# Kernel tuning notes

Hardware: AMD Instinct MI355X
Metric: run time of the kernel (lower is better)

## Reference

```python
import jax, jax.numpy as jnp
import numpy as np


def conv(x, w, b=None, pad=1):
    y = jax.lax.conv_general_dilated(x, w, (1, 1), [(pad, pad), (pad, pad)],
                                     dimension_numbers=('NCHW', 'OIHW', 'NCHW'))
    if b is not None:
        y = y + b[None, :, None, None]
    return y


def grid_sample(img, gx, gy):
    # bilinear, zeros padding, align_corners=False (torch F.grid_sample default)
    B, C, H, W = img.shape
    ix = ((gx + 1.0) * W - 1.0) * 0.5
    iy = ((gy + 1.0) * H - 1.0) * 0.5
    x0 = jnp.floor(ix)
    y0 = jnp.floor(iy)

    def gather(xi, yi):
        valid = (xi >= 0) & (xi <= W - 1) & (yi >= 0) & (yi <= H - 1)
        xc = jnp.clip(xi, 0, W - 1).astype(jnp.int32)
        yc = jnp.clip(yi, 0, H - 1).astype(jnp.int32)
        b = jnp.arange(B)[:, None, None]
        return img[b, :, yc, xc] * valid[..., None].astype(img.dtype)  # (B,H,W,C)

    wx1 = ix - x0
    wy1 = iy - y0
    wx0 = 1.0 - wx1
    wy0 = 1.0 - wy1
    out = (gather(x0, y0) * (wx0 * wy0)[..., None]
           + gather(x0 + 1, y0) * (wx1 * wy0)[..., None]
           + gather(x0, y0 + 1) * (wx0 * wy1)[..., None]
           + gather(x0 + 1, y0 + 1) * (wx1 * wy1)[..., None])
    return out.transpose(0, 3, 1, 2)  # (B,C,H,W)


def setup_inputs() -> dict:
    key = jax.random.key(0)
    ks = jax.random.split(key, 32)
    B, H, W, hd = 4, 512, 512, 16
    f = lambda k, shp: jax.random.normal(k, shp, dtype=jnp.float32) * 0.05
    z = lambda n: jnp.zeros((n,), dtype=jnp.float32)
    d = {
        'net': f(ks[0], (B, hd, H, W)),
        'inp': f(ks[1], (B, hd, H, W)),
        'corr': f(ks[2], (B, 3, H, W)),
        'noise': f(ks[3], (B, 3, H, W)),
        # BasicMotionEncoder (channels=3, hidden=32, output_dim=64)
        'wc1': f(ks[4], (32, 3, 3, 3)), 'bc1': z(32),
        'wc2': f(ks[5], (32, 32, 3, 3)), 'bc2': z(32),
        'wf1': f(ks[6], (32, 3, 3, 3)), 'bf1': z(32),
        'wf2': f(ks[7], (32, 32, 3, 3)), 'bf2': z(32),
        'we': f(ks[8], (61, 64, 3, 3)), 'be': z(61),
        # SepConvGRU (hidden_size=16, L=4)
        'loc1_w': f(ks[9], (16, 96, 5, 5)), 'loc1_b': z(16),
        'loc2_w': f(ks[10], (8, 16, 5, 5)), 'loc2_b': z(8),
        'wz': f(ks[11], (16, 144, 3, 3)), 'bz': z(16),
        'wr': f(ks[12], (16, 144, 3, 3)), 'br': z(16),
        'wq': f(ks[13], (16, 96, 3, 3)), 'bq': z(16),
        # CBAM (reduction 16 -> mid=1; bias-free, standard impl)
        'ca_w1': f(ks[14], (1, 16, 1, 1)),
        'ca_w2': f(ks[15], (16, 1, 1, 1)),
        'sa_w': f(ks[16], (1, 2, 7, 7)),
        # FlowHead (input 16, hidden 64, out 3)
        'fh1_w': f(ks[17], (64, 16, 3, 3)), 'fh1_b': z(64),
        'fh2_w': f(ks[18], (3, 64, 3, 3)), 'fh2_b': z(3),
    }
    return d


def reference(net, inp, corr, noise, wc1, bc1, wc2, bc2, wf1, bf1, wf2, bf2, we, be,
              loc1_w, loc1_b, loc2_w, loc2_b, wz, bz, wr, br, wq, bq,
              ca_w1, ca_w2, sa_w, fh1_w, fh1_b, fh2_w, fh2_b):
    # --- BasicMotionEncoder ---
    cor = jax.nn.relu(conv(corr, wc1, bc1, 1))
    cor = jax.nn.relu(conv(cor, wc2, bc2, 1))
    flo = jax.nn.relu(conv(noise, wf1, bf1, 1))
    flo = jax.nn.relu(conv(flo, wf2, bf2, 1))
    mo = jax.nn.relu(conv(jnp.concatenate([cor, flo], 1), we, be, 1))
    motion = jnp.concatenate([mo, noise], 1)  # (B,64,H,W)
    x = jnp.concatenate([inp, motion], 1)     # (B,hd+64,H,W)
    h = net
    B, C, H, W = h.shape
    # --- SepConvGRU ---
    t = jax.nn.leaky_relu(conv(jnp.concatenate([x, h], 1), loc1_w, loc1_b, 2), 0.2)
    flows = conv(t, loc2_w, loc2_b, 2)        # (B,2L,H,W)
    L = flows.shape[1] // 2
    flows = flows.reshape(B, L, 2, H, W)
    xx = jnp.arange(W, dtype=h.dtype)[None, None, :]  # (1,1,W)
    yy = jnp.arange(H, dtype=h.dtype)[None, :, None]  # (1,H,1)

    def warp_one(flow):  # flow: (B,2,H,W); warp h by -flow
        vgx = xx - flow[:, 0]
        vgy = yy - flow[:, 1]
        gx = 2.0 * vgx / max(W - 1, 1) - 1.0
        gy = 2.0 * vgy / max(H - 1, 1) - 1.0
        return grid_sample(h, gx, gy)

    wrapped = jax.vmap(warp_one, in_axes=1, out_axes=1)(flows)  # (B,L,C,H,W)
    wrapped = wrapped.reshape(B, L * C, H, W)
    hx = jnp.concatenate([wrapped, x], 1)     # (B,9*hd,H,W)
    zg = jax.nn.sigmoid(conv(hx, wz, bz, 1))
    rg = jax.nn.sigmoid(conv(hx, wr, br, 1))
    q = jnp.tanh(conv(jnp.concatenate([rg * h, x], 1), wq, bq, 1))
    h = (1.0 - zg) * h + zg * q
    # --- CBAM ---
    avg = h.mean((2, 3), keepdims=True)
    mx = h.max((2, 3), keepdims=True)
    mlp = lambda v: conv(jax.nn.relu(conv(v, ca_w1, None, 0)), ca_w2, None, 0)
    h = h * jax.nn.sigmoid(mlp(avg) + mlp(mx))
    sa = jnp.concatenate([h.mean(1, keepdims=True), h.max(1, keepdims=True)], 1)
    h = h * jax.nn.sigmoid(conv(sa, sa_w, None, 3))
    # --- FlowHead ---
    delta_flow = conv(jax.nn.relu(conv(h, fh1_w, fh1_b, 1)), fh2_w, fh2_b, 1)
    return h, delta_flow
```

## Files before the change

### kernel.cpp

```cpp
#include <hip/hip_runtime.h>
#include <hip/hip_bf16.h>
#include <math.h>

using bf16 = __hip_bfloat16;
typedef __attribute__((ext_vector_type(8))) short short8;
typedef __attribute__((ext_vector_type(4))) float f32x4;

__device__ __forceinline__ float b2f(bf16 v){ return __bfloat162float(v); }
__device__ __forceinline__ bf16 f2b(float v){ return __float2bfloat16(v); }
__device__ __forceinline__ float bs2f(short s){
  union{unsigned u; float f;} x; x.u = ((unsigned)(unsigned short)s)<<16; return x.f;
}
__device__ __forceinline__ float lo16(unsigned u){ union{unsigned x; float f;} v; v.x = u<<16;          return v.f; }
__device__ __forceinline__ float hi16(unsigned u){ union{unsigned x; float f;} v; v.x = u & 0xffff0000u; return v.f; }
__device__ __forceinline__ unsigned cvt_pk_bf16(float lo, float hi){
  unsigned r; asm("v_cvt_pk_bf16_f32 %0, %1, %2" : "=v"(r) : "v"(lo), "v"(hi)); return r;
}
__device__ __forceinline__ float hw_exp2(float x){ float r; asm("v_exp_f32 %0, %1" : "=v"(r) : "v"(x)); return r; }
__device__ __forceinline__ float hw_rcp(float x){ float r; asm("v_rcp_f32 %0, %1" : "=v"(r) : "v"(x)); return r; }
__device__ __forceinline__ float fast_sigmoid(float v){ return hw_rcp(1.f + hw_exp2(v * -1.44269504f)); }
__device__ __forceinline__ float fast_tanh(float v){ return 1.f - 2.f*hw_rcp(1.f + hw_exp2(v * 2.88539008f)); }

template<int A> __device__ __forceinline__ float act_fn(float v){
  if constexpr (A==1) return fmaxf(v, 0.f);
  else if constexpr (A==2) return v > 0.f ? v : 0.2f*v;
  else if constexpr (A==3) return fast_sigmoid(v);
  else if constexpr (A==4) return fast_tanh(v);
  else return v;
}

struct Srcs9 { const bf16* p[9]; int code[9]; };

template<int KK, int ACT, int NT>
__global__ __launch_bounds__(256) void conv_mfma(
    Srcs9 S, int Gin, const bf16* __restrict__ flows,
    const bf16* __restrict__ Bw, const float* __restrict__ bias,
    bf16* __restrict__ outS, size_t slabS, float* __restrict__ outF, int Cout,
    int H, int W)
{
  constexpr int TS=16, HALO=TS+KK-1, PAD=KK/2, NPAIR=(KK*KK+1)/2, HH=HALO*HALO;
  constexpr int CP=24, CPB=48;
  constexpr int NMT = (NT==1)?4:((NT==2)?8:16);
  __shared__ __align__(16) bf16 As[HH*CP];
  const int tid=threadIdx.x, lane=tid&63, wv=tid>>6;
  const int ln=lane&15, gq=lane>>4;
  const int tilesx=W/TS;
  const int nwg = gridDim.x, cpx = nwg >> 3;
  const int bidx = (blockIdx.x & 7)*cpx + (blockIdx.x >> 3);
  const int tx0 = (bidx % tilesx)*TS, ty0 = (bidx / tilesx)*TS;
  const int b=blockIdx.z; const int HW=H*W;
  int ntile, mt0;
  if constexpr (NT==1){ ntile=0;    mt0=wv*4; }
  else if constexpr (NT==2){ ntile=wv&1; mt0=(wv>>1)*8; }
  else { ntile=wv; mt0=0; }

  f32x4 acc[NMT];
  #pragma unroll
  for (int t=0;t<NMT;++t) acc[t]=(f32x4){0.f,0.f,0.f,0.f};

  const short8 Z8 = {0,0,0,0,0,0,0,0};
  const int px0=tid, px1=tid+256;
  const int hy0=px0/HALO, hx0=px0-hy0*HALO;
  const int hy1=px1/HALO, hx1=px1-hy1*HALO;
  const bool act1 = (px1<HH);
  const int gy0=ty0+hy0-PAD, gx0=tx0+hx0-PAD;
  const int gy1=ty0+hy1-PAD, gx1=tx0+hx1-PAD;
  const bool in0 = (gy0>=0&&gy0<H&&gx0>=0&&gx0<W);
  const bool in1 = act1 && (gy1>=0&&gy1<H&&gx1>=0&&gx1<W);
  const size_t po0 = ((size_t)b*HW + (size_t)(in0?gy0:0)*W + (in0?gx0:0))*16;
  const size_t po1 = ((size_t)b*HW + (size_t)(in1?gy1:0)*W + (in1?gx1:0))*16;

  auto gather = [&](int g, bool inb, size_t po, int gy, int gx, short8& A0, short8& A1){
    const int code = S.code[g];
    const bf16* sp = S.p[g];
    if (code == 0) {
      if (inb) {
        const bf16* qp = sp + po;
        A0 = *(const short8*)qp; A1 = *(const short8*)(qp+8);
      } else { A0 = Z8; A1 = Z8; }
    } else {
      if (inb) {
        const int l = code-1;
        const unsigned fp_ = *(const unsigned*)(flows + po + 2*l);
        const float fx = lo16(fp_), fy = hi16(fp_);
        const float vgx = (float)gx - fx, vgy = (float)gy - fy;
        const float gxn = 2.f*vgx/(float)(W-1) - 1.f;
        const float gyn = 2.f*vgy/(float)(H-1) - 1.f;
        const float ix = ((gxn+1.f)*(float)W - 1.f)*0.5f;
        const float iy = ((gyn+1.f)*(float)H - 1.f)*0.5f;
        const float x0f = floorf(ix), y0f = floorf(iy);
        const float wx1 = ix-x0f, wy1 = iy-y0f, wx0 = 1.f-wx1, wy0 = 1.f-wy1;
        const int x0=(int)x0f, y0=(int)y0f, x1=x0+1, y1=y0+1;
        const bool vx0=(x0>=0)&(x0<W), vx1=(x1>=0)&(x1<W);
        const bool vy0=(y0>=0)&(y0<H), vy1=(y1>=0)&(y1<H);
        const int xc0=min(max(x0,0),W-1), xc1=min(max(x1,0),W-1);
        const int yc0=min(max(y0,0),H-1), yc1=min(max(y1,0),H-1);
        const float w00=wx0*wy0*((vx0&&vy0)?1.f:0.f);
        const float w10=wx1*wy0*((vx1&&vy0)?1.f:0.f);
        const float w01=wx0*wy1*((vx0&&vy1)?1.f:0.f);
        const float w11=wx1*wy1*((vx1&&vy1)?1.f:0.f);
        const bf16* nb = sp + (size_t)b*HW*16;
        const bf16* p00 = nb + ((size_t)yc0*W+xc0)*16;
        const bf16* p10 = nb + ((size_t)yc0*W+xc1)*16;
        const bf16* p01 = nb + ((size_t)yc1*W+xc0)*16;
        const bf16* p11 = nb + ((size_t)yc1*W+xc1)*16;
        unsigned t00[8], t10[8], t01[8], t11[8], od[8];
        *(uint4*)t00     = *(const uint4*)p00; *(uint4*)(t00+4) = *(const uint4*)(p00+8);
        *(uint4*)t10     = *(const uint4*)p10; *(uint4*)(t10+4) = *(const uint4*)(p10+8);
        *(uint4*)t01     = *(const uint4*)p01; *(uint4*)(t01+4) = *(const uint4*)(p01+8);
        *(uint4*)t11     = *(const uint4*)p11; *(uint4*)(t11+4) = *(const uint4*)(p11+8);
        #pragma unroll
        for (int j=0;j<8;++j){
          const float lo = w00*lo16(t00[j]) + w10*lo16(t10[j]) + w01*lo16(t01[j]) + w11*lo16(t11[j]);
          const float hi = w00*hi16(t00[j]) + w10*hi16(t10[j]) + w01*hi16(t01[j]) + w11*hi16(t11[j]);
          od[j] = cvt_pk_bf16(lo, hi);
        }
        A0 = *(const short8*)od; A1 = *(const short8*)(od+4);
      } else { A0 = Z8; A1 = Z8; }
    }
  };

  auto mfma_g = [&](int g){
    const bf16* bw = Bw + ((size_t)g*NPAIR*NT + ntile)*512;
    const char* bufm = (const char*)As + (size_t)mt0*(HALO*CPB);
    #pragma unroll
    for (int p=0;p<NPAIR;++p){
      const short8 bfrag = *(const short8*)(bw + (size_t)p*(NT*512) + lane*8);
      int off = 2*p + (gq>>1);
      if (off >= KK*KK) off = 0;
      const int dy = off/KK, dx = off - (off/KK)*KK;
      const int ce = (dy*HALO + ln + dx)*CPB + ((gq&1)<<4);
      #pragma unroll
      for (int t=0;t<NMT;++t){
        const short8 af = *(const short8*)(bufm + (size_t)t*(HALO*CPB) + ce);
        acc[t] = __builtin_amdgcn_mfma_f32_16x16x32_bf16(af, bfrag, acc[t], 0, 0, 0);
      }
    }
  };

  for (int g=0; g<Gin; ++g) {
    short8 a0, a1, c0v, c1v;
    gather(g, in0, po0, gy0, gx0, a0, a1);
    if (act1) gather(g, in1, po1, gy1, gx1, c0v, c1v);
    if (g > 0) { mfma_g(g-1); __syncthreads(); }
    *(short8*)(As + (size_t)px0*CP)     = a0;
    *(short8*)(As + (size_t)px0*CP + 8) = a1;
    if (act1){
      *(short8*)(As + (size_t)px1*CP)     = c0v;
      *(short8*)(As + (size_t)px1*CP + 8) = c1v;
    }
    __syncthreads();
  }
  mfma_g(Gin-1);

  const int co = ntile*16 + ln;
  const float bv = bias[co];
  if (outS) {
    #pragma unroll
    for (int t=0;t<NMT;++t){
      const int y = ty0 + mt0 + t;
      bf16* op = outS + (size_t)ntile*slabS + ((size_t)b*HW + (size_t)y*W + tx0 + gq*4)*16 + ln;
      const float f0 = act_fn<ACT>(acc[t][0] + bv);
      const float f1 = act_fn<ACT>(acc[t][1] + bv);
      const float f2 = act_fn<ACT>(acc[t][2] + bv);
      const float f3 = act_fn<ACT>(acc[t][3] + bv);
      const unsigned p01 = cvt_pk_bf16(f0, f1), p23 = cvt_pk_bf16(f2, f3);
      unsigned short* os = (unsigned short*)op;
      os[0]  = (unsigned short)p01; os[16] = (unsigned short)(p01>>16);
      os[32] = (unsigned short)p23; os[48] = (unsigned short)(p23>>16);
    }
  } else {
    if (co < Cout) {
      #pragma unroll
      for (int t=0;t<NMT;++t){
        const int y = ty0 + mt0 + t;
        float4 f;
        f.x = act_fn<ACT>(acc[t][0]+bv); f.y = act_fn<ACT>(acc[t][1]+bv);
        f.z = act_fn<ACT>(acc[t][2]+bv); f.w = act_fn<ACT>(acc[t][3]+bv);
        *(float4*)(outF + ((size_t)b*Cout + co)*HW + (size_t)y*W + tx0 + gq*4) = f;
      }
    }
  }
}

struct PrepDesc {
  const float *W1, *W2, *b1, *b2;
  int coSplit, NPAIR, NTp, Cout, CinO, T;
  int lo0, hi0, d2, lo2, hi2;
  int base[9];
  int total;
};
struct PrepAll { PrepDesc d[10]; int n; };

__global__ void prep_w(PrepAll P, bf16* __restrict__ Bw, float* __restrict__ bOut, int grand){
  const int i = blockIdx.x*256 + threadIdx.x;
  if (i < P.n*64) {
    const int c=i>>6, t=i&63; const PrepDesc& D=P.d[c];
    float bv=0.f;
    if (t < D.Cout) bv = (!D.b2 || t < D.coSplit) ? D.b1[t] : D.b2[t-D.coSplit];
    bOut[c*64+t]=bv;
  }
  if (i >= grand) return;
  int c=0, off0=0;
  while (i >= off0 + P.d[c].total) { off0 += P.d[c].total; ++c; }
  const PrepDesc& D = P.d[c];
  const int j = i - off0;
  const int jj=j&7, l=(j>>3)&63, ln2=l&15, gq2=l>>4;
  int r=j>>9; const int nt=r%D.NTp; r/=D.NTp; const int p=r%D.NPAIR; const int g=r/D.NPAIR;
  const int k=gq2*8+jj, off=2*p+(k>>4), ci=k&15, co=nt*16+ln2;
  float w=0.f;
  if (off<D.T && co<D.Cout) {
    const int lo = (g==0)?D.lo0:0, hi=(g==0)?D.hi0:16;
    if (!D.W2 || co < D.coSplit) {
      if (ci>=lo && ci<hi) w = D.W1[((size_t)co*D.CinO + D.base[g]+ci)*D.T + off];
    } else {
      if (ci>=D.lo2 && ci<D.hi2) w = D.W2[((size_t)(co-D.coSplit)*D.CinO + D.base[g]+ci+D.d2)*D.T + off];
    }
  }
  Bw[i] = f2b(w);
}

__global__ void pack_all(const float* __restrict__ corr, const float* __restrict__ noise,
                         const float* __restrict__ inp, const float* __restrict__ net,
                         bf16* __restrict__ cnoise, bf16* __restrict__ inpT,
                         bf16* __restrict__ netT, int HW){
  const int px = blockIdx.x*256+threadIdx.x; const int b=blockIdx.y;
  if (px>=HW) return;
  const size_t base = ((size_t)b*HW+px)*16;
  __align__(16) bf16 t[16];
  #pragma unroll
  for (int c=0;c<16;++c) t[c]=f2b(0.f);
  #pragma unroll
  for (int c=0;c<3;++c){
    t[c]   = f2b(corr [((size_t)b*3+c)*HW+px]);
    t[3+c] = f2b(noise[((size_t)b*3+c)*HW+px]);
  }
  *(short8*)(cnoise+base) = *(const short8*)t; *(short8*)(cnoise+base+8) = *(const short8*)(t+8);
  #pragma unroll
  for (int c=0;c<16;++c) t[c]=f2b(inp[((size_t)b*16+c)*HW+px]);
  *(short8*)(inpT+base) = *(const short8*)t; *(short8*)(inpT+base+8) = *(const short8*)(t+8);
  #pragma unroll
  for (int c=0;c<16;++c) t[c]=f2b(net[((size_t)b*16+c)*HW+px]);
  *(short8*)(netT+base) = *(const short8*)t; *(short8*)(netT+base+8) = *(const short8*)(t+8);
}

__global__ void noise_tail(const float* __restrict__ noise, bf16* __restrict__ mslab3, int HW){
  const int px = blockIdx.x*256+threadIdx.x; const int b=blockIdx.y;
  if (px>=HW) return;
  bf16* d = mslab3 + ((size_t)b*HW+px)*16;
  #pragma unroll
  for (int c=0;c<3;++c) d[13+c] = f2b(noise[((size_t)b*3+c)*HW+px]);
}

__global__ void rh_k(const bf16* __restrict__ rg, const bf16* __restrict__ netT,
                     bf16* __restrict__ rh, int HW){
  const int px = blockIdx.x*256+threadIdx.x; const int b=blockIdx.y;
  if (px>=HW) return;
  const size_t base = ((size_t)b*HW+px)*16;
  const short8 r0=*(const short8*)(rg+base),  r1=*(const short8*)(rg+base+8);
  const short8 n0=*(const short8*)(netT+base), n1=*(const short8*)(netT+base+8);
  __align__(16) bf16 t[16];
  #pragma unroll
  for (int c=0;c<8;++c){
    t[c]   = f2b(bs2f(r0[c])*bs2f(n0[c]));
    t[8+c] = f2b(bs2f(r1[c])*bs2f(n1[c]));
  }
  *(short8*)(rh+base) = *(const short8*)t; *(short8*)(rh+base+8) = *(const short8*)(t+8);
}

__global__ void h1_k(const bf16* __restrict__ zg, const bf16* __restrict__ q,
                     const float* __restrict__ net, bf16* __restrict__ hT, int HW){
  const int px = blockIdx.x*256+threadIdx.x; const int b=blockIdx.y;
  if (px>=HW) return;
  const size_t base = ((size_t)b*HW+px)*16;
  const short8 z0=*(const short8*)(zg+base), z1=*(const short8*)(zg+base+8);
  const short8 q0=*(const short8*)(q+base),  q1=*(const short8*)(q+base+8);
  __align__(16) bf16 t[16];
  #pragma unroll
  for (int c=0;c<8;++c){
    const float za=bs2f(z0[c]), zb=bs2f(z1[c]);
    const float na=net[((size_t)b*16+c)*HW+px], nb2=net[((size_t)b*16+8+c)*HW+px];
    t[c]   = f2b((1.f-za)*na + za*bs2f(q0[c]));
    t[8+c] = f2b((1.f-zb)*nb2 + zb*bs2f(q1[c]));
  }
  *(short8*)(hT+base) = *(const short8*)t; *(short8*)(hT+base+8) = *(const short8*)(t+8);
}

__global__ __launch_bounds__(256) void castats_p1(const bf16* __restrict__ hT,
                                                  float* __restrict__ part, int HW){
  const int blk=blockIdx.x, b=blockIdx.y;
  const int per = HW>>5;
  const bf16* base = hT + ((size_t)b*HW + (size_t)blk*per)*16;
  float s[16], m[16];
  #pragma unroll
  for (int c=0;c<16;++c){ s[c]=0.f; m[c]=-3.4e38f; }
  for (int i=threadIdx.x;i<per;i+=256){
    const short8 a=*(const short8*)(base+(size_t)i*16);
    const short8 bb=*(const short8*)(base+(size_t)i*16+8);
    #pragma unroll
    for (int c=0;c<8;++c){
      const float v=bs2f(a[c]);  s[c]+=v;   m[c]=fmaxf(m[c],v);
      const float w=bs2f(bb[c]); s[8+c]+=w; m[8+c]=fmaxf(m[8+c],w);
    }
  }
  #pragma unroll
  for (int o=32;o>=1;o>>=1){
    #pragma unroll
    for (int c=0;c<16;++c){ s[c]+=__shfl_down(s[c],o); m[c]=fmaxf(m[c],__shfl_down(m[c],o)); }
  }
  __shared__ float ls[4][16], lm[4][16];
  const int w4=threadIdx.x>>6;
  if ((threadIdx.x&63)==0){
    #pragma unroll
    for (int c=0;c<16;++c){ ls[w4][c]=s[c]; lm[w4][c]=m[c]; }
  }
  __syncthreads();
  if (threadIdx.x<16){
    const int c=threadIdx.x;
    part[((size_t)(b*32+blk))*32 + c]      = ls[0][c]+ls[1][c]+ls[2][c]+ls[3][c];
    part[((size_t)(b*32+blk))*32 + 16 + c] = fmaxf(fmaxf(lm[0][c],lm[1][c]),fmaxf(lm[2][c],lm[3][c]));
  }
}

__global__ void castats_fin(const float* __restrict__ part, const float* __restrict__ w1,
                            const float* __restrict__ w2, float* __restrict__ scale, int HW){
  const int t = threadIdx.x; if (t>=64) return;
  const int b=t>>4, c=t&15;
  float s=0.f, m=-3.4e38f;
  for (int k=0;k<32;++k){
    s += part[((size_t)(b*32+k))*32 + c];
    m  = fmaxf(m, part[((size_t)(b*32+k))*32 + 16 + c]);
  }
  float pa = w1[c]*(s/(float)HW), pm = w1[c]*m;
  #pragma unroll
  for (int o=8;o>=1;o>>=1){ pa += __shfl_xor(pa,o,16); pm += __shfl_xor(pm,o,16); }
  const float y = w2[c]*fmaxf(pa,0.f) + w2[c]*fmaxf(pm,0.f);
  scale[t] = fast_sigmoid(y);
}

__global__ void sastats_k(const bf16* __restrict__ hT, const float* __restrict__ scale,
                          bf16* __restrict__ sa2, int HW){
  const int px = blockIdx.x*256+threadIdx.x; const int b=blockIdx.y;
  if (px>=HW) return;
  const size_t base = ((size_t)b*HW+px)*16;
  const short8 a=*(const short8*)(hT+base), c8=*(const short8*)(hT+base+8);
  float s=0.f, m=-3.4e38f;
  #pragma unroll
  for (int c=0;c<8;++c){
    const float v=bs2f(a[c])*scale[b*16+c];    s+=v; m=fmaxf(m,v);
    const float w=bs2f(c8[c])*scale[b*16+8+c]; s+=w; m=fmaxf(m,w);
  }
  sa2[((size_t)b*2+0)*HW+px] = f2b(s*(1.f/16.f));
  sa2[((size_t)b*2+1)*HW+px] = f2b(m);
}

__global__ __launch_bounds__(256) void hfinal2(bf16* __restrict__ hT, const float* __restrict__ scale,
    const bf16* __restrict__ sa2, const float* __restrict__ saw,
    float* __restrict__ outh, int H, int W){
  __shared__ float wl[98];
  if (threadIdx.x < 98) wl[threadIdx.x] = saw[threadIdx.x];
  __syncthreads();
  const int i = blockIdx.x*256 + threadIdx.x; const int b = blockIdx.y;
  const int HW = H*W;
  if (i >= HW) return;
  const int y = i / W, x = i - (i/W)*W;
  float s = 0.f;
  #pragma unroll
  for (int ch=0; ch<2; ++ch){
    const size_t base = ((size_t)b*2+ch)*HW;
    for (int ky=0;ky<7;++ky){
      const int yy=y+ky-3; if (yy<0||yy>=H) continue;
      for (int kx=0;kx<7;++kx){
        const int xx=x+kx-3; if (xx<0||xx>=W) continue;
        s += b2f(sa2[base+(size_t)yy*W+xx]) * wl[ch*49+ky*7+kx];
      }
    }
  }
  const float sa = fast_sigmoid(s);
  const size_t base = ((size_t)b*HW+i)*16;
  const short8 a=*(const short8*)(hT+base), c8=*(const short8*)(hT+base+8);
  __align__(16) bf16 t[16];
  #pragma unroll
  for (int c=0;c<8;++c){
    const float v=bs2f(a[c])*scale[b*16+c]*sa;
    const float w=bs2f(c8[c])*scale[b*16+8+c]*sa;
    t[c]=f2b(v); t[8+c]=f2b(w);
    outh[((size_t)b*16+c)*HW+i]=v; outh[((size_t)b*16+8+c)*HW+i]=w;
  }
  *(short8*)(hT+base)=*(const short8*)t; *(short8*)(hT+base+8)=*(const short8*)(t+8);
}

extern "C" void kernel_launch(void* const* d_in, const int* in_sizes, int n_in,
                              void* d_out, int out_size, void* d_ws, size_t ws_size,
                              hipStream_t stream)
{
  const float* net   = (const float*)d_in[0];
  const float* inp   = (const float*)d_in[1];
  const float* corr  = (const float*)d_in[2];
  const float* noise = (const float*)d_in[3];
  const float* wc1 = (const float*)d_in[4];  const float* bc1 = (const float*)d_in[5];
  const float* wc2 = (const float*)d_in[6];  const float* bc2 = (const float*)d_in[7];
  const float* wf1 = (const float*)d_in[8];  const float* bf1 = (const float*)d_in[9];
  const float* wf2 = (const float*)d_in[10]; const float* bf2 = (const float*)d_in[11];
  const float* we  = (const float*)d_in[12]; const float* be  = (const float*)d_in[13];
  const float* loc1_w = (const float*)d_in[14]; const float* loc1_b = (const float*)d_in[15];
  const float* loc2_w = (const float*)d_in[16]; const float* loc2_b = (const float*)d_in[17];
  const float* wz = (const float*)d_in[18]; const float* bz = (const float*)d_in[19];
  const float* wr = (const float*)d_in[20]; const float* br = (const float*)d_in[21];
  const float* wq = (const float*)d_in[22]; const float* bq = (const float*)d_in[23];
  const float* ca_w1 = (const float*)d_in[24]; const float* ca_w2 = (const float*)d_in[25];
  const float* sa_w  = (const float*)d_in[26];
  const float* fh1_w = (const float*)d_in[27]; const float* fh1_b = (const float*)d_in[28];
  const float* fh2_w = (const float*)d_in[29]; const float* fh2_b = (const float*)d_in[30];

  const int B = 4, H = 512, W = 512, HW = H*W;
  const size_t U  = 32ull<<20;
  const size_t SS = (size_t)B*HW*16;
  char* ws = (char*)d_ws;

  bf16* cor1   = (bf16*)(ws + 0*U);
  bf16* flo1   = (bf16*)(ws + 2*U);
  bf16* motion = (bf16*)(ws + 0*U);
  bf16* fh1o   = (bf16*)(ws + 0*U);
  bf16* inpT   = (bf16*)(ws + 4*U);
  bf16* flo2   = (bf16*)(ws + 5*U);
  bf16* flows  = (bf16*)(ws + 5*U);
  bf16* qb     = (bf16*)(ws + 5*U);
  bf16* cnoise = (bf16*)(ws + 6*U);
  bf16* tbuf   = (bf16*)(ws + 6*U);
  bf16* rh     = (bf16*)(ws + 6*U);
  bf16* hT     = (bf16*)(ws + 6*U);
  bf16* netT   = (bf16*)(ws + 7*U);
  float* part    = (float*)(ws + 4*U);
  float* scale   = (float*)(ws + 4*U + (64<<10));
  bf16*  sa2     = (bf16*)(ws + 4*U + (1<<20));
  bf16*  Bw_fh2  = (bf16*)(ws + 4*U + (16<<20));
  float* bias_fh2= (float*)(ws + 4*U + (17<<20));

  float* out_h  = (float*)d_out;
  float* out_df = out_h + (size_t)B*16*HW;
  bf16*  zgrg   = (bf16*)d_out;
  bf16*  BwAll  = (bf16*)out_df;
  float* biasAll= (float*)(BwAll + 190464);

  const size_t oMrg=0, oCor2=10240, oFlo2=20480, oMo=30720, oLoc1=71680,
               oLoc2=111616, oZgrg=118272, oQ=164352, oFh1=179712;
  const int grand = 189952;

  const dim3 pgrid((HW+255)/256, B);
  const dim3 cgrid((W/16)*(H/16), 1, B);

  auto mk = [](const float* W1, const float* W2, int coSplit, const float* b1, const float* b2,
               int G, int NP, int NTp, int Cout, int CinO, int T,
               int lo0, int hi0, int d2, int lo2, int hi2,
               int b0,int b1_,int b2_,int b3,int b4,int b5,int b6,int b7,int b8)->PrepDesc{
    PrepDesc d{};
    d.W1=W1; d.W2=W2; d.b1=b1; d.b2=b2; d.coSplit=coSplit;
    d.NPAIR=NP; d.NTp=NTp; d.Cout=Cout; d.CinO=CinO; d.T=T;
    d.lo0=lo0; d.hi0=hi0; d.d2=d2; d.lo2=lo2; d.hi2=hi2;
    const int bs[9]={b0,b1_,b2_,b3,b4,b5,b6,b7,b8};
    for (int g=0;g<9;++g) d.base[g]=bs[g];
    d.total = G*NP*NTp*512;
    return d;
  };

  {
    PrepAll P{}; P.n = 9;
    P.d[0] = mk(wc1, wf1, 32, bc1, bf1, 1,5,4, 64,3,9,  0,3, -3,3,6, 0,0,0,0,0,0,0,0,0);
    P.d[1] = mk(wc2, nullptr,0, bc2,nullptr, 2,5,2, 32,32,9, 0,16, 0,0,16, 0,16,0,0,0,0,0,0,0);
    P.d[2] = mk(wf2, nullptr,0, bf2,nullptr, 2,5,2, 32,32,9, 0,16, 0,0,16, 0,16,0,0,0,0,0,0,0);
    P.d[3] = mk(we,  nullptr,0, be, nullptr, 4,5,4, 61,64,9, 0,16, 0,0,16, 0,16,32,48,0,0,0,0,0);
    P.d[4] = mk(loc1_w,nullptr,0, loc1_b,nullptr, 6,13,1, 16,96,25, 0,16, 0,0,16, 0,16,32,48,64,80,0,0,0);
    P.d[5] = mk(loc2_w,nullptr,0, loc2_b,nullptr, 1,13,1, 8,16,25,  0,16, 0,0,16, 0,0,0,0,0,0,0,0,0);
    P.d[6] = mk(wz, wr, 16, bz, br, 9,5,2, 32,144,9, 0,16, 0,0,16, 0,16,32,48,64,80,96,112,128);
    P.d[7] = mk(wq, nullptr,0, bq, nullptr, 6,5,1, 16,96,9, 0,16, 0,0,16, 0,16,32,48,64,80,0,0,0);
    P.d[8] = mk(fh1_w,nullptr,0, fh1_b,nullptr, 1,5,4, 64,16,9, 0,16, 0,0,16, 0,0,0,0,0,0,0,0,0);
    prep_w<<<(grand+255)/256,256,0,stream>>>(P, BwAll, biasAll, grand);
  }

  pack_all<<<pgrid,256,0,stream>>>(corr, noise, inp, net, cnoise, inpT, netT, HW);

  { Srcs9 S{}; S.p[0]=cnoise;
    conv_mfma<3,1,4><<<cgrid,256,0,stream>>>(S,1,nullptr,BwAll+oMrg,biasAll+0*64,cor1,SS,nullptr,64,H,W); }
  { Srcs9 S{}; S.p[0]=cor1; S.p[1]=cor1+SS;
    conv_mfma<3,1,2><<<cgrid,256,0,stream>>>(S,2,nullptr,BwAll+oCor2,biasAll+1*64,zgrg,SS,nullptr,32,H,W); }
  { Srcs9 S{}; S.p[0]=flo1; S.p[1]=flo1+SS;
    conv_mfma<3,1,2><<<cgrid,256,0,stream>>>(S,2,nullptr,BwAll+oFlo2,biasAll+2*64,flo2,SS,nullptr,32,H,W); }
  { Srcs9 S{}; S.p[0]=zgrg; S.p[1]=zgrg+SS; S.p[2]=flo2; S.p[3]=flo2+SS;
    conv_mfma<3,1,4><<<cgrid,256,0,stream>>>(S,4,nullptr,BwAll+oMo,biasAll+3*64,motion,SS,nullptr,61,H,W); }
  noise_tail<<<pgrid,256,0,stream>>>(noise, motion+3*SS, HW);

  { Srcs9 S{}; S.p[0]=inpT; S.p[1]=motion; S.p[2]=motion+SS; S.p[3]=motion+2*SS; S.p[4]=motion+3*SS; S.p[5]=netT;
    conv_mfma<5,2,1><<<cgrid,256,0,stream>>>(S,6,nullptr,BwAll+oLoc1,biasAll+4*64,tbuf,SS,nullptr,16,H,W); }
  { Srcs9 S{}; S.p[0]=tbuf;
    conv_mfma<5,0,1><<<cgrid,256,0,stream>>>(S,1,nullptr,BwAll+oLoc2,biasAll+5*64,flows,SS,nullptr,8,H,W); }

  { Srcs9 S{};
    S.p[0]=netT; S.code[0]=1; S.p[1]=netT; S.code[1]=2;
    S.p[2]=netT; S.code[2]=3; S.p[3]=netT; S.code[3]=4;
    S.p[4]=inpT; S.p[5]=motion; S.p[6]=motion+SS; S.p[7]=motion+2*SS; S.p[8]=motion+3*SS;
    conv_mfma<3,3,2><<<cgrid,256,0,stream>>>(S,9,flows,BwAll+oZgrg,biasAll+6*64,zgrg,SS,nullptr,32,H,W); }
  rh_k<<<pgrid,256,0,stream>>>(zgrg+SS, netT, rh, HW);
  { Srcs9 S{}; S.p[0]=rh; S.p[1]=inpT; S.p[2]=motion; S.p[3]=motion+SS; S.p[4]=motion+2*SS; S.p[5]=motion+3*SS;
    conv_mfma<3,4,1><<<cgrid,256,0,stream>>>(S,6,nullptr,BwAll+oQ,biasAll+7*64,qb,SS,nullptr,16,H,W); }
  h1_k<<<pgrid,256,0,stream>>>(zgrg, qb, net, hT, HW);

  { PrepAll P{}; P.n = 1;
    P.d[0] = mk(fh2_w,nullptr,0, fh2_b,nullptr, 4,5,1, 3,64,9, 0,16, 0,0,16, 0,16,32,48,0,0,0,0,0);
    prep_w<<<(10240+255)/256,256,0,stream>>>(P, Bw_fh2, bias_fh2, 10240); }

  castats_p1<<<dim3(32,B),256,0,stream>>>(hT, part, HW);
  castats_fin<<<1,64,0,stream>>>(part, ca_w1, ca_w2, scale, HW);
  sastats_k<<<pgrid,256,0,stream>>>(hT, scale, sa2, HW);
  hfinal2<<<pgrid,256,0,stream>>>(hT, scale, sa2, sa_w, out_h, H, W);

  { Srcs9 S{}; S.p[0]=hT;
    conv_mfma<3,1,4><<<cgrid,256,0,stream>>>(S,1,nullptr,BwAll+oFh1,biasAll+8*64,fh1o,SS,nullptr,64,H,W); }
  { Srcs9 S{}; S.p[0]=fh1o; S.p[1]=fh1o+SS; S.p[2]=fh1o+2*SS; S.p[3]=fh1o+3*SS;
    conv_mfma<3,0,1><<<cgrid,256,0,stream>>>(S,4,nullptr,Bw_fh2,bias_fh2,nullptr,SS,out_df,3,H,W); }
}
```

Measured before the change: 896.4 us.

## Fuse r*h into q-conv gather, merge weight prep with packing, read bf16 net

Removes the standalone rh_k kernel by adding a gather mode that multiplies the reset gate by the hidden state while loading the q-conv input halo. Merges the weight-prep and input-pack kernels into one launch that uses an extra grid row. h1_k now reads the packed bf16 net instead of strided fp32 net. This saves launches and one full-resolution write/read round trip, at the cost of recomputing the product for halo pixels and slightly different rounding of net in h1.

```diff
diff --git a/kernel.cpp b/kernel.cpp
--- a/kernel.cpp
+++ b/kernel.cpp
@@ -33,7 +33,7 @@
 
 template<int KK, int ACT, int NT>
 __global__ __launch_bounds__(256) void conv_mfma(
-    Srcs9 S, int Gin, const bf16* __restrict__ flows,
+    Srcs9 S, int Gin, const bf16* __restrict__ flows, const bf16* __restrict__ rgp,
     const bf16* __restrict__ Bw, const float* __restrict__ bias,
     bf16* __restrict__ outS, size_t slabS, float* __restrict__ outF, int Cout,
     int H, int W)
@@ -77,6 +77,16 @@
       if (inb) {
         const bf16* qp = sp + po;
         A0 = *(const short8*)qp; A1 = *(const short8*)(qp+8);
+      } else { A0 = Z8; A1 = Z8; }
+    } else if (code == 5) {
+      if (inb) {
+        unsigned nu[8], ru[8], od[8];
+        *(uint4*)nu     = *(const uint4*)(sp + po);  *(uint4*)(nu+4) = *(const uint4*)(sp + po + 8);
+        *(uint4*)ru     = *(const uint4*)(rgp + po); *(uint4*)(ru+4) = *(const uint4*)(rgp + po + 8);
+        #pragma unroll
+        for (int j=0;j<8;++j)
+          od[j] = cvt_pk_bf16(lo16(nu[j])*lo16(ru[j]), hi16(nu[j])*hi16(ru[j]));
+        A0 = *(const short8*)od; A1 = *(const short8*)(od+4);
       } else { A0 = Z8; A1 = Z8; }
     } else {
       if (inb) {
@@ -192,8 +202,8 @@
 };
 struct PrepAll { PrepDesc d[10]; int n; };
 
-__global__ void prep_w(PrepAll P, bf16* __restrict__ Bw, float* __restrict__ bOut, int grand){
-  const int i = blockIdx.x*256 + threadIdx.x;
+__device__ __forceinline__ void prep_body(const PrepAll& P, bf16* Bw, float* bOut,
+                                          int grand, int i){
   if (i < P.n*64) {
     const int c=i>>6, t=i&63; const PrepDesc& D=P.d[c];
     float bv=0.f;
@@ -220,11 +230,19 @@
   Bw[i] = f2b(w);
 }
 
-__global__ void pack_all(const float* __restrict__ corr, const float* __restrict__ noise,
-                         const float* __restrict__ inp, const float* __restrict__ net,
-                         bf16* __restrict__ cnoise, bf16* __restrict__ inpT,
-                         bf16* __restrict__ netT, int HW){
-  const int px = blockIdx.x*256+threadIdx.x; const int b=blockIdx.y;
+__global__ void prep_w(PrepAll P, bf16* __restrict__ Bw, float* __restrict__ bOut, int grand){
+  prep_body(P, Bw, bOut, grand, blockIdx.x*256 + threadIdx.x);
+}
+
+__global__ void prep_pack(PrepAll P, bf16* __restrict__ Bw, float* __restrict__ bOut, int grand,
+                          const float* __restrict__ corr, const float* __restrict__ noise,
+                          const float* __restrict__ inp, const float* __restrict__ net,
+                          bf16* __restrict__ cnoise, bf16* __restrict__ inpT,
+                          bf16* __restrict__ netT, int HW)
+{
+  const int b = blockIdx.y;
+  if (b >= 4) { prep_body(P, Bw, bOut, grand, blockIdx.x*256 + threadIdx.x); return; }
+  const int px = blockIdx.x*256+threadIdx.x;
   if (px>=HW) return;
   const size_t base = ((size_t)b*HW+px)*16;
   __align__(16) bf16 t[16];
@@ -252,36 +270,20 @@
   for (int c=0;c<3;++c) d[13+c] = f2b(noise[((size_t)b*3+c)*HW+px]);
 }
 
-__global__ void rh_k(const bf16* __restrict__ rg, const bf16* __restrict__ netT,
-                     bf16* __restrict__ rh, int HW){
-  const int px = blockIdx.x*256+threadIdx.x; const int b=blockIdx.y;
-  if (px>=HW) return;
-  const size_t base = ((size_t)b*HW+px)*16;
-  const short8 r0=*(const short8*)(rg+base),  r1=*(const short8*)(rg+base+8);
-  const short8 n0=*(const short8*)(netT+base), n1=*(const short8*)(netT+base+8);
-  __align__(16) bf16 t[16];
-  #pragma unroll
-  for (int c=0;c<8;++c){
-    t[c]   = f2b(bs2f(r0[c])*bs2f(n0[c]));
-    t[8+c] = f2b(bs2f(r1[c])*bs2f(n1[c]));
-  }
-  *(short8*)(rh+base) = *(const short8*)t; *(short8*)(rh+base+8) = *(const short8*)(t+8);
-}
-
 __global__ void h1_k(const bf16* __restrict__ zg, const bf16* __restrict__ q,
-                     const float* __restrict__ net, bf16* __restrict__ hT, int HW){
+                     const bf16* __restrict__ netT, bf16* __restrict__ hT, int HW){
   const int px = blockIdx.x*256+threadIdx.x; const int b=blockIdx.y;
   if (px>=HW) return;
   const size_t base = ((size_t)b*HW+px)*16;
   const short8 z0=*(const short8*)(zg+base), z1=*(const short8*)(zg+base+8);
   const short8 q0=*(const short8*)(q+base),  q1=*(const short8*)(q+base+8);
+  const short8 n0=*(const short8*)(netT+base), n1=*(const short8*)(netT+base+8);
   __align__(16) bf16 t[16];
   #pragma unroll
   for (int c=0;c<8;++c){
     const float za=bs2f(z0[c]), zb=bs2f(z1[c]);
-    const float na=net[((size_t)b*16+c)*HW+px], nb2=net[((size_t)b*16+8+c)*HW+px];
-    t[c]   = f2b((1.f-za)*na + za*bs2f(q0[c]));
-    t[8+c] = f2b((1.f-zb)*nb2 + zb*bs2f(q1[c]));
+    t[c]   = f2b((1.f-za)*bs2f(n0[c]) + za*bs2f(q0[c]));
+    t[8+c] = f2b((1.f-zb)*bs2f(n1[c]) + zb*bs2f(q1[c]));
   }
   *(short8*)(hT+base) = *(const short8*)t; *(short8*)(hT+base+8) = *(const short8*)(t+8);
 }
@@ -428,7 +430,6 @@
   bf16* qb     = (bf16*)(ws + 5*U);
   bf16* cnoise = (bf16*)(ws + 6*U);
   bf16* tbuf   = (bf16*)(ws + 6*U);
-  bf16* rh     = (bf16*)(ws + 6*U);
   bf16* hT     = (bf16*)(ws + 6*U);
   bf16* netT   = (bf16*)(ws + 7*U);
   float* part    = (float*)(ws + 4*U);
@@ -475,35 +476,35 @@
     P.d[6] = mk(wz, wr, 16, bz, br, 9,5,2, 32,144,9, 0,16, 0,0,16, 0,16,32,48,64,80,96,112,128);
     P.d[7] = mk(wq, nullptr,0, bq, nullptr, 6,5,1, 16,96,9, 0,16, 0,0,16, 0,16,32,48,64,80,0,0,0);
     P.d[8] = mk(fh1_w,nullptr,0, fh1_b,nullptr, 1,5,4, 64,16,9, 0,16, 0,0,16, 0,0,0,0,0,0,0,0,0);
-    prep_w<<<(grand+255)/256,256,0,stream>>>(P, BwAll, biasAll, grand);
-  }
-
-  pack_all<<<pgrid,256,0,stream>>>(corr, noise, inp, net, cnoise, inpT, netT, HW);
+    prep_pack<<<dim3((HW+255)/256, B+1),256,0,stream>>>(P, BwAll, biasAll, grand,
+        corr, noise, inp, net, cnoise, inpT, netT, HW);
+  }
 
   { Srcs9 S{}; S.p[0]=cnoise;
-    conv_mfma<3,1,4><<<cgrid,256,0,stream>>>(S,1,nullptr,BwAll+oMrg,biasAll+0*64,cor1,SS,nullptr,64,H,W); }
+    conv_mfma<3,1,4><<<cgrid,256,0,stream>>>(S,1,nullptr,nullptr,BwAll+oMrg,biasAll+0*64,cor1,SS,nullptr,64,H,W); }
   { Srcs9 S{}; S.p[0]=cor1; S.p[1]=cor1+SS;
-    conv_mfma<3,1,2><<<cgrid,256,0,stream>>>(S,2,nullptr,BwAll+oCor2,biasAll+1*64,zgrg,SS,nullptr,32,H,W); }
+    conv_mfma<3,1,2><<<cgrid,256,0,stream>>>(S,2,nullptr,nullptr,BwAll+oCor2,biasAll+1*64,zgrg,SS,nullptr,32,H,W); }
   { Srcs9 S{}; S.p[0]=flo1; S.p[1]=flo1+SS;
-    conv_mfma<3,1,2><<<cgrid,256,0,stream>>>(S,2,nullptr,BwAll+oFlo2,biasAll+2*64,flo2,SS,nullptr,32,H,W); }
+    conv_mfma<3,1,2><<<cgrid,256,0,stream>>>(S,2,nullptr,nullptr,BwAll+oFlo2,biasAll+2*64,flo2,SS,nullptr,32,H,W); }
   { Srcs9 S{}; S.p[0]=zgrg; S.p[1]=zgrg+SS; S.p[2]=flo2; S.p[3]=flo2+SS;
-    conv_mfma<3,1,4><<<cgrid,256,0,stream>>>(S,4,nullptr,BwAll+oMo,biasAll+3*64,motion,SS,nullptr,61,H,W); }
+    conv_mfma<3,1,4><<<cgrid,256,0,stream>>>(S,4,nullptr,nullptr,BwAll+oMo,biasAll+3*64,motion,SS,nullptr,61,H,W); }
   noise_tail<<<pgrid,256,0,stream>>>(noise, motion+3*SS, HW);
 
   { Srcs9 S{}; S.p[0]=inpT; S.p[1]=motion; S.p[2]=motion+SS; S.p[3]=motion+2*SS; S.p[4]=motion+3*SS; S.p[5]=netT;
-    conv_mfma<5,2,1><<<cgrid,256,0,stream>>>(S,6,nullptr,BwAll+oLoc1,biasAll+4*64,tbuf,SS,nullptr,16,H,W); }
+    conv_mfma<5,2,1><<<cgrid,256,0,stream>>>(S,6,nullptr,nullptr,BwAll+oLoc1,biasAll+4*64,tbuf,SS,nullptr,16,H,W); }
   { Srcs9 S{}; S.p[0]=tbuf;
-    conv_mfma<5,0,1><<<cgrid,256,0,stream>>>(S,1,nullptr,BwAll+oLoc2,biasAll+5*64,flows,SS,nullptr,8,H,W); }
+    conv_mfma<5,0,1><<<cgrid,256,0,stream>>>(S,1,nullptr,nullptr,BwAll+oLoc2,biasAll+5*64,flows,SS,nullptr,8,H,W); }
 
   { Srcs9 S{};
     S.p[0]=netT; S.code[0]=1; S.p[1]=netT; S.code[1]=2;
     S.p[2]=netT; S.code[2]=3; S.p[3]=netT; S.code[3]=4;
     S.p[4]=inpT; S.p[5]=motion; S.p[6]=motion+SS; S.p[7]=motion+2*SS; S.p[8]=motion+3*SS;
-    conv_mfma<3,3,2><<<cgrid,256,0,stream>>>(S,9,flows,BwAll+oZgrg,biasAll+6*64,zgrg,SS,nullptr,32,H,W); }
-  rh_k<<<pgrid,256,0,stream>>>(zgrg+SS, netT, rh, HW);
-  { Srcs9 S{}; S.p[0]=rh; S.p[1]=inpT; S.p[2]=motion; S.p[3]=motion+SS; S.p[4]=motion+2*SS; S.p[5]=motion+3*SS;
-    conv_mfma<3,4,1><<<cgrid,256,0,stream>>>(S,6,nullptr,BwAll+oQ,biasAll+7*64,qb,SS,nullptr,16,H,W); }
-  h1_k<<<pgrid,256,0,stream>>>(zgrg, qb, net, hT, HW);
+    conv_mfma<3,3,2><<<cgrid,256,0,stream>>>(S,9,flows,nullptr,BwAll+oZgrg,biasAll+6*64,zgrg,SS,nullptr,32,H,W); }
+  { Srcs9 S{};
+    S.p[0]=netT; S.code[0]=5;
+    S.p[1]=inpT; S.p[2]=motion; S.p[3]=motion+SS; S.p[4]=motion+2*SS; S.p[5]=motion+3*SS;
+    conv_mfma<3,4,1><<<cgrid,256,0,stream>>>(S,6,nullptr,zgrg+SS,BwAll+oQ,biasAll+7*64,qb,SS,nullptr,16,H,W); }
+  h1_k<<<pgrid,256,0,stream>>>(zgrg, qb, netT, hT, HW);
 
   { PrepAll P{}; P.n = 1;
     P.d[0] = mk(fh2_w,nullptr,0, fh2_b,nullptr, 4,5,1, 3,64,9, 0,16, 0,0,16, 0,16,32,48,0,0,0,0,0);
@@ -515,7 +516,7 @@
   hfinal2<<<pgrid,256,0,stream>>>(hT, scale, sa2, sa_w, out_h, H, W);
 
   { Srcs9 S{}; S.p[0]=hT;
-    conv_mfma<3,1,4><<<cgrid,256,0,stream>>>(S,1,nullptr,BwAll+oFh1,biasAll+8*64,fh1o,SS,nullptr,64,H,W); }
+    conv_mfma<3,1,4><<<cgrid,256,0,stream>>>(S,1,nullptr,nullptr,BwAll+oFh1,biasAll+8*64,fh1o,SS,nullptr,64,H,W); }
   { Srcs9 S{}; S.p[0]=fh1o; S.p[1]=fh1o+SS; S.p[2]=fh1o+2*SS; S.p[3]=fh1o+3*SS;
-    conv_mfma<3,0,1><<<cgrid,256,0,stream>>>(S,4,nullptr,Bw_fh2,bias_fh2,nullptr,SS,out_df,3,H,W); }
-}
+    conv_mfma<3,0,1><<<cgrid,256,0,stream>>>(S,4,nullptr,nullptr,Bw_fh2,bias_fh2,nullptr,SS,out_df,3,H,W); }
+}
```

Result: slower. 933.2 us (+4.1%).
